# Kernel tuning notes

Measured on AMD Instinct MI355X. Metric: run time of the kernel, lower is better.

The kernel has to match this reference:

```python
import jax, jax.numpy as jnp
import numpy as np

B, S, D = 2, 2048, 2048
H, KVH, HD = 16, 4, 128
M = 2  # modalities
THETA = 10000.0
REP = H // KVH


def make_freq_cis(seq_len, head_dim, theta):
    # (S, head_dim//2, 2, 2) rotation matrices [[cos,-sin],[sin,cos]]
    inv = theta ** (-jnp.arange(0, head_dim, 2, dtype=jnp.float32) / head_dim)
    ang = jnp.arange(seq_len, dtype=jnp.float32)[:, None] * inv[None, :]  # (S, hd/2)
    c, s = jnp.cos(ang), jnp.sin(ang)
    row0 = jnp.stack([c, -s], axis=-1)
    row1 = jnp.stack([s, c], axis=-1)
    return jnp.stack([row0, row1], axis=-2)  # (S, hd/2, 2, 2)


def setup_inputs() -> dict:
    key = jax.random.key(0)
    ks = jax.random.split(key, 7)
    std = D ** -0.5
    x = jax.random.normal(ks[0], (B, S, D), dtype=jnp.float32)
    freq_cis = make_freq_cis(S, HD, THETA)
    modality_ids = jax.random.randint(ks[1], (B, S), 0, M, dtype=jnp.int32)
    wq = jax.random.normal(ks[2], (M, D, H * HD), dtype=jnp.float32) * std
    wk = jax.random.normal(ks[3], (M, D, KVH * HD), dtype=jnp.float32) * std
    wv = jax.random.normal(ks[4], (M, D, KVH * HD), dtype=jnp.float32) * std
    wo = jax.random.normal(ks[5], (M, H * HD, D), dtype=jnp.float32) * std
    return {"x": x, "freq_cis": freq_cis, "modality_ids": modality_ids,
            "wq": wq, "wk": wk, "wv": wv, "wo": wo}


def apply_rope(t, freq_cis):
    # t: (B, S, h, HD); freq_cis: (S, HD//2, 2, 2)
    b, s, h, hd = t.shape
    t2 = t.reshape(b, s, h, hd // 2, 2)
    out = jnp.einsum('bshdk,sdjk->bshdj', t2, freq_cis)
    return out.reshape(b, s, h, hd)


def reference(x, freq_cis, modality_ids, wq, wk, wv, wo):
    bsz, seq, dim = x.shape
    onehot = jax.nn.one_hot(modality_ids, M, dtype=x.dtype)  # (B,S,M)
    # per-modality QKV projection, then combine (masks partition tokens)
    q = jnp.einsum('bsm,bsd,mdo->bso', onehot, x, wq).reshape(bsz, seq, H, HD)
    k = jnp.einsum('bsm,bsd,mdo->bso', onehot, x, wk).reshape(bsz, seq, KVH, HD)
    v = jnp.einsum('bsm,bsd,mdo->bso', onehot, x, wv).reshape(bsz, seq, KVH, HD)
    q = apply_rope(q, freq_cis)
    k = apply_rope(k, freq_cis)
    # GQA: repeat_interleave kv heads along head dim
    k = jnp.repeat(k, REP, axis=2)
    v = jnp.repeat(v, REP, axis=2)
    scale = 1.0 / jnp.sqrt(jnp.asarray(HD, dtype=x.dtype))
    scores = jnp.einsum('bqhd,bkhd->bhqk', q, k) * scale
    causal = jnp.tril(jnp.ones((seq, seq), dtype=bool))
    scores = jnp.where(causal[None, None], scores, jnp.finfo(x.dtype).min)
    probs = jax.nn.softmax(scores, axis=-1)
    attn = jnp.einsum('bhqk,bkhd->bqhd', probs, v).reshape(bsz, seq, H * HD)
    # per-modality output projection
    out = jnp.einsum('bsm,bso,moe->bse', onehot, attn, wo)
    return out
```

## Files before the change

kernel.cpp:

```cpp
#include <hip/hip_runtime.h>
#include <stdint.h>

typedef unsigned short u16;
typedef __bf16  bf16x8 __attribute__((ext_vector_type(8), may_alias));
typedef u16     u16x8  __attribute__((ext_vector_type(8), may_alias));
typedef float   f32x4  __attribute__((ext_vector_type(4)));
typedef float   f32x4u __attribute__((ext_vector_type(4), may_alias));

#define Bv   2
#define Sv   2048
#define Dv   2048
#define Hv   16
#define KVHv 4
#define HDv  128
#define Tv   (Bv*Sv)
#define QKVN 3072
#define MAXROWS 4352

__device__ __forceinline__ float b2f(u16 u) {
    union { float f; uint32_t i; } x; x.i = ((uint32_t)u) << 16; return x.f;
}
__device__ __forceinline__ u16 f2b(float f) {
    union { float f; uint32_t u; } x; x.f = f;
    uint32_t r = x.u + 0x7fff + ((x.u >> 16) & 1);
    return (u16)(r >> 16);
}
__device__ __forceinline__ void gload_lds16(const void* g, void* l) {
    __builtin_amdgcn_global_load_lds((__attribute__((address_space(1))) void*)(uintptr_t)g,
                                     (__attribute__((address_space(3))) void*)(uintptr_t)l,
                                     16, 0, 0);
}

__global__ __launch_bounds__(1024) void scan_mod(const int* __restrict__ mod, int* __restrict__ fwd,
                                                 int* __restrict__ inv, int* __restrict__ hdr) {
    __shared__ int cnt[1024];
    const int tid = threadIdx.x;
    int m[4]; int c = 0;
#pragma unroll
    for (int e = 0; e < 4; ++e) { m[e] = mod[tid * 4 + e]; c += (m[e] == 0); }
    cnt[tid] = c;
    __syncthreads();
    for (int off = 1; off < 1024; off <<= 1) {
        int v = (tid >= off) ? cnt[tid - off] : 0;
        __syncthreads();
        cnt[tid] += v;
        __syncthreads();
    }
    const int c0 = cnt[1023];
    const int c0pad = (c0 + 255) & ~255;
    const int c1 = Tv - c0;
    const int total = c0pad + ((c1 + 255) & ~255);
    for (int p = tid; p < MAXROWS; p += 1024) inv[p] = -1;
    __syncthreads();
    const int ex0 = cnt[tid] - c;
    int z = 0;
#pragma unroll
    for (int e = 0; e < 4; ++e) {
        int t = tid * 4 + e;
        int pos;
        if (m[e] == 0) { pos = ex0 + z; ++z; }
        else           { pos = c0pad + (t - (ex0 + z)); }
        fwd[t] = pos;
        inv[pos] = t;
    }
    if (tid == 0) { hdr[0] = total >> 8; hdr[1] = c0pad; hdr[2] = total; }
}

__global__ void gather_cast(const float* __restrict__ x, const int* __restrict__ inv,
                            u16* __restrict__ Xg) {
    int v = blockIdx.x * 256 + threadIdx.x;
    int pos = v >> 8, c8 = (v & 255) * 8;
    int t = inv[pos];
    u16x8 val = {0, 0, 0, 0, 0, 0, 0, 0};
    if (t >= 0) {
        f32x4u a = *(const f32x4u*)&x[(size_t)t * Dv + c8];
        f32x4u b = *(const f32x4u*)&x[(size_t)t * Dv + c8 + 4];
#pragma unroll
        for (int j = 0; j < 4; ++j) { val[j] = f2b(a[j]); val[4 + j] = f2b(b[j]); }
    }
    *(u16x8*)&Xg[(size_t)pos * Dv + c8] = val;
}

__global__ void transpose_cast(const float* __restrict__ in, u16* __restrict__ out, int C,
                               size_t inZ, size_t outZ) {
    in  += (size_t)blockIdx.z * inZ;
    out += (size_t)blockIdx.z * outZ;
    __shared__ u16 tile[64][72];
    const int tr = blockIdx.y * 64, tc = blockIdx.x * 64;
    const int tid = threadIdx.x;
#pragma unroll
    for (int i = 0; i < 4; ++i) {
        int s = tid + 256 * i;
        int r = s >> 4, c4 = (s & 15) * 4;
        f32x4u v = *(const f32x4u*)&in[(size_t)(tr + r) * C + tc + c4];
#pragma unroll
        for (int j = 0; j < 4; ++j) tile[r][c4 + j] = f2b(v[j]);
    }
    __syncthreads();
#pragma unroll
    for (int i = 0; i < 2; ++i) {
        int s = tid + 256 * i;
        int r = s >> 3, c8 = (s & 7) * 8;
        u16x8 v;
#pragma unroll
        for (int j = 0; j < 8; ++j) v[j] = tile[c8 + j][r];
        *(u16x8*)&out[(size_t)(tc + r) * 2048 + tr + c8] = v;
    }
}

__device__ __forceinline__ void store_c(u16* C, size_t idx, float v) { C[idx] = f2b(v); }
__device__ __forceinline__ void store_c(float* C, size_t idx, float v) { C[idx] = v; }

template <typename OutT>
__global__ __launch_bounds__(512, 2) void gemm256(const u16* __restrict__ A,
                                                  const u16* __restrict__ Bt,
                                                  OutT* __restrict__ C,
                                                  const int* __restrict__ inv,
                                                  const int* __restrict__ hdr,
                                                  int Nfull, int ldC) {
    const int total = hdr[2], c0pad = hdr[1];
    const int bm = blockIdx.y * 256;
    if (bm >= total) return;
    const u16* B = Bt + (size_t)((bm >= c0pad) ? 1 : 0) * Nfull * 2048;
    const int bn = blockIdx.x * 256;
    const int tid = threadIdx.x;
    const int wave = tid >> 6, lane = tid & 63;
    const int l15 = lane & 15, l4 = lane >> 4;
    const int wm = wave >> 2;
    const int wn = wave & 3;
    const int bhh = wn >> 1, brr = (wn & 1) * 64;
    const int rsw = l15 & 7;
    __shared__ u16 ldsA[2][2][128 * 64];
    __shared__ u16 ldsB[2][2][128 * 64];
    const int srow = tid >> 3;
    const int ssw  = (tid & 7) ^ (srow & 7);
    const int wofs = wave * 8 * 64;

    f32x4 acc[8][4] = {};

    auto stA = [&](int sl, int h, int jrb, int kt) {
        gload_lds16(A + (size_t)(bm + h * 128 + jrb * 64 + srow) * 2048 + kt * 64 + ssw * 8,
                    &ldsA[sl][h][jrb * 64 * 64 + wofs]);
    };
    auto stB = [&](int sl, int h, int jrb, int kt) {
        gload_lds16(B + (size_t)(bn + h * 128 + jrb * 64 + srow) * 2048 + kt * 64 + ssw * 8,
                    &ldsB[sl][h][jrb * 64 * 64 + wofs]);
    };

    stB(0, 0, 0, 0); stB(0, 0, 1, 0); stB(0, 1, 0, 0); stB(0, 1, 1, 0);
    stA(0, 0, 0, 0); stA(0, 1, 0, 0); stA(0, 0, 1, 0); stA(0, 1, 1, 0);
    asm volatile("s_waitcnt vmcnt(2)" ::: "memory");
    __builtin_amdgcn_s_barrier();
    __builtin_amdgcn_sched_barrier(0);

    for (int kt = 0; kt < 32; ++kt) {
        const int s = kt & 1;
        const bool st = (kt < 31);
        bf16x8 bfr[4][2];
#pragma unroll
        for (int fj = 0; fj < 4; ++fj)
#pragma unroll
            for (int kc = 0; kc < 2; ++kc)
                bfr[fj][kc] = *(const bf16x8*)&ldsB[s][bhh][(brr + fj * 16 + l15) * 64 + ((kc * 4 + l4) ^ rsw) * 8];
#pragma unroll
        for (int q = 0; q < 4; ++q) {
            bf16x8 af[2][2];
#pragma unroll
            for (int fi = 0; fi < 2; ++fi)
#pragma unroll
                for (int kc = 0; kc < 2; ++kc)
                    af[fi][kc] = *(const bf16x8*)&ldsA[s][wm][(q * 32 + fi * 16 + l15) * 64 + ((kc * 4 + l4) ^ rsw) * 8];
            if (st) {
                if      (q == 0) { stB(s ^ 1, 0, 0, kt + 1); stB(s ^ 1, 0, 1, kt + 1); }
                else if (q == 1) { stB(s ^ 1, 1, 0, kt + 1); stB(s ^ 1, 1, 1, kt + 1); }
                else if (q == 2) { stA(s ^ 1, 0, 0, kt + 1); stA(s ^ 1, 1, 0, kt + 1); }
                else             { stA(s ^ 1, 0, 1, kt + 1); stA(s ^ 1, 1, 1, kt + 1); }
            }
            __builtin_amdgcn_s_setprio(1);
#pragma unroll
            for (int kc = 0; kc < 2; ++kc)
#pragma unroll
                for (int fi = 0; fi < 2; ++fi)
#pragma unroll
                    for (int fj = 0; fj < 4; ++fj)
                        acc[q * 2 + fi][fj] = __builtin_amdgcn_mfma_f32_16x16x32_bf16(
                            af[fi][kc], bfr[fj][kc], acc[q * 2 + fi][fj], 0, 0, 0);
            __builtin_amdgcn_s_setprio(0);
            if (q == 1) {
                if (st) asm volatile("s_waitcnt vmcnt(4)" ::: "memory");
                else    asm volatile("s_waitcnt vmcnt(0)" ::: "memory");
                __builtin_amdgcn_sched_barrier(0);
            }
            if (q == 3 && st) {
                asm volatile("s_waitcnt vmcnt(2)" ::: "memory");
                __builtin_amdgcn_sched_barrier(0);
            }
            __builtin_amdgcn_s_barrier();
            __builtin_amdgcn_sched_barrier(0);
        }
    }
#pragma unroll
    for (int fi = 0; fi < 8; ++fi)
#pragma unroll
        for (int r = 0; r < 4; ++r) {
            int row = bm + wm * 128 + fi * 16 + l4 * 4 + r;
            int t = inv[row];
            if (t >= 0) {
#pragma unroll
                for (int fj = 0; fj < 4; ++fj) {
                    int col = bn + wn * 64 + fj * 16 + l15;
                    store_c(C, (size_t)t * ldC + col, acc[fi][fj][r]);
                }
            }
        }
}

__global__ void rope_kernel(u16* __restrict__ QKV, const float* __restrict__ fc) {
    int p8 = blockIdx.x * 256 + threadIdx.x;
    const int t = p8 / 160;
    const int r8 = (p8 - t * 160) * 8;
    const int s = t & (Sv - 1);
    int col, d2b; float scale;
    if (r8 < 1024) { col = 2 * r8;               d2b = r8 & 63;  scale = 0.12751742f; }
    else           { int rr = r8 - 1024; col = 2048 + 2 * rr; d2b = rr & 63; scale = 1.0f; }
    u16* ptr = QKV + (size_t)t * QKVN + col;
    u16x8 va = *(const u16x8*)ptr;
    u16x8 vb = *(const u16x8*)(ptr + 8);
    u16 arr[16];
#pragma unroll
    for (int i = 0; i < 8; ++i) { arr[i] = va[i]; arr[8 + i] = vb[i]; }
#pragma unroll
    for (int i = 0; i < 8; ++i) {
        float t0 = b2f(arr[2 * i]), t1 = b2f(arr[2 * i + 1]);
        f32x4u f = *(const f32x4u*)&fc[((size_t)s * 64 + d2b + i) * 4];
        arr[2 * i]     = f2b((t0 * f[0] + t1 * f[1]) * scale);
        arr[2 * i + 1] = f2b((t0 * f[2] + t1 * f[3]) * scale);
    }
#pragma unroll
    for (int i = 0; i < 8; ++i) { va[i] = arr[i]; vb[i] = arr[8 + i]; }
    *(u16x8*)ptr = va;
    *(u16x8*)(ptr + 8) = vb;
}

__global__ __launch_bounds__(512) void attn_fwd(const u16* __restrict__ QKV, u16* __restrict__ Ag,
                                                const int* __restrict__ fwd) {
    const int p = blockIdx.x;
    const int h = blockIdx.y, b = blockIdx.z;
    const int kvh = h >> 2;
    const int tid = threadIdx.x, wave = tid >> 6, lane = tid & 63;
    const int wgrp = wave >> 2, wl = wave & 3;
    const int l15 = lane & 15, l4 = lane >> 4;
    const int myqb = wgrp ? (31 - p) : p;
    __shared__ u16 smem[32768];

    bf16x8 qf[4];
    {
        const size_t qrow = (size_t)(b * Sv + myqb * 64 + wl * 16 + l15);
#pragma unroll
        for (int kc = 0; kc < 4; ++kc)
            qf[kc] = *(const bf16x8*)&QKV[qrow * QKVN + h * 128 + kc * 32 + l4 * 8];
    }
    f32x4 oacc[8] = {};
    float mrow = -1e30f;
    float lrow = 0.f;

    const size_t kvbase = (size_t)b * Sv * QKVN + 2048 + kvh * 128;

    {
#pragma unroll
        for (int i = 0; i < 2; ++i) {
            int s_u = wave * 64 + 512 * i;
            int s = s_u + lane;
            int r = s >> 4;
            int kvsrc = (r & 32) | ((r & 12) << 1) | ((r & 16) >> 2) | (r & 3);
            int cs = (s & 15) ^ (r & 7);
            gload_lds16(QKV + kvbase + (size_t)kvsrc * QKVN + cs * 8, &smem[(size_t)s_u * 8]);
        }
        u16x8 vr0 = *(const u16x8*)&QKV[kvbase + 512 + (size_t)lane * QKVN + (0 * 8 + wave) * 8];
        u16x8 vr1 = *(const u16x8*)&QKV[kvbase + 512 + (size_t)lane * QKVN + (1 * 8 + wave) * 8];
#pragma unroll
        for (int jj = 0; jj < 8; ++jj) {
            int d0 = wave * 8 + jj, d1 = (8 + wave) * 8 + jj;
            smem[16384 + d0 * 64 + ((((lane >> 3) ^ jj) << 3) | (lane & 7))] = vr0[jj];
            smem[16384 + d1 * 64 + ((((lane >> 3) ^ jj) << 3) | (lane & 7))] = vr1[jj];
        }
    }
    __syncthreads();

    for (int j = 0; j < 32; ++j) {
        const int cur = j & 1;
        const bool stage_next = (j < 31);
        u16* Kcur = smem + cur * 8192;
        u16* Knxt = smem + (cur ^ 1) * 8192;
        u16* Vcur = smem + 16384 + cur * 8192;
        u16* Vnxt = smem + 16384 + (cur ^ 1) * 8192;
        u16x8 vn0, vn1;
        if (stage_next) {
            const size_t nb = kvbase + (size_t)(j + 1) * 64 * QKVN;
#pragma unroll
            for (int i = 0; i < 2; ++i) {
                int s_u = wave * 64 + 512 * i;
                int s = s_u + lane;
                int r = s >> 4;
                int kvsrc = (r & 32) | ((r & 12) << 1) | ((r & 16) >> 2) | (r & 3);
                int cs = (s & 15) ^ (r & 7);
                gload_lds16(QKV + nb + (size_t)kvsrc * QKVN + cs * 8, &Knxt[(size_t)s_u * 8]);
            }
            vn0 = *(const u16x8*)&QKV[nb + 512 + (size_t)lane * QKVN + (0 * 8 + wave) * 8];
            vn1 = *(const u16x8*)&QKV[nb + 512 + (size_t)lane * QKVN + (1 * 8 + wave) * 8];
        }
        if (j <= myqb) {
            f32x4 sacc[4] = {};
            __builtin_amdgcn_s_setprio(1);
#pragma unroll
            for (int kc = 0; kc < 4; ++kc)
#pragma unroll
                for (int nt = 0; nt < 4; ++nt) {
                    int cs = ((kc * 4 + l4) ^ (l15 & 7));
                    bf16x8 kf = *(const bf16x8*)&Kcur[(nt * 16 + l15) * 128 + cs * 8];
                    sacc[nt] = __builtin_amdgcn_mfma_f32_16x16x32_bf16(kf, qf[kc], sacc[nt], 0, 0, 0);
                }
            __builtin_amdgcn_s_setprio(0);
            if (j == myqb) {
#pragma unroll
                for (int nt = 0; nt < 4; ++nt)
#pragma unroll
                    for (int r = 0; r < 4; ++r)
                        if ((nt >> 1) * 32 + l4 * 8 + (nt & 1) * 4 + r > wl * 16 + l15)
                            sacc[nt][r] = -1e30f;
            }
            f32x4 mv = sacc[0];
#pragma unroll
            for (int nt = 1; nt < 4; ++nt)
#pragma unroll
                for (int r = 0; r < 4; ++r) mv[r] = fmaxf(mv[r], sacc[nt][r]);
            float mx = fmaxf(fmaxf(mv[0], mv[1]), fmaxf(mv[2], mv[3]));
            mx = fmaxf(mx, __shfl_xor(mx, 16, 64));
            mx = fmaxf(mx, __shfl_xor(mx, 32, 64));
            const bool defer = __all(mx <= mrow + 8.0f);
            if (!defer) {
                float mnew = fmaxf(mrow, mx);
                float fs = exp2f(mrow - mnew);
                mrow = mnew;
                lrow *= fs;
#pragma unroll
                for (int nt = 0; nt < 8; ++nt)
#pragma unroll
                    for (int r = 0; r < 4; ++r) oacc[nt][r] *= fs;
            }
            f32x4 pv = {0.f, 0.f, 0.f, 0.f};
#pragma unroll
            for (int nt = 0; nt < 4; ++nt)
#pragma unroll
                for (int r = 0; r < 4; ++r) {
                    float pe = exp2f(sacc[nt][r] - mrow);
                    sacc[nt][r] = pe;
                    pv[r] += pe;
                }
            float ps = (pv[0] + pv[1]) + (pv[2] + pv[3]);
            ps += __shfl_xor(ps, 16, 64);
            ps += __shfl_xor(ps, 32, 64);
            lrow += ps;
            union { uint32_t w[4]; bf16x8 v; } pb0u, pb1u;
#pragma unroll
            for (int nt = 0; nt < 2; ++nt) {
                asm("v_cvt_pk_bf16_f32 %0, %1, %2" : "=v"(pb0u.w[nt * 2])     : "v"(sacc[nt][0]), "v"(sacc[nt][1]));
                asm("v_cvt_pk_bf16_f32 %0, %1, %2" : "=v"(pb0u.w[nt * 2 + 1]) : "v"(sacc[nt][2]), "v"(sacc[nt][3]));
                asm("v_cvt_pk_bf16_f32 %0, %1, %2" : "=v"(pb1u.w[nt * 2])     : "v"(sacc[nt + 2][0]), "v"(sacc[nt + 2][1]));
                asm("v_cvt_pk_bf16_f32 %0, %1, %2" : "=v"(pb1u.w[nt * 2 + 1]) : "v"(sacc[nt + 2][2]), "v"(sacc[nt + 2][3]));
            }
            bf16x8 pb0 = pb0u.v, pb1 = pb1u.v;
            __builtin_amdgcn_s_setprio(1);
#pragma unroll
            for (int nt = 0; nt < 8; ++nt) {
                int d = nt * 16 + l15;
                bf16x8 v0 = *(const bf16x8*)&Vcur[d * 64 + ((l4 ^ (l15 & 7)) << 3)];
                bf16x8 v1 = *(const bf16x8*)&Vcur[d * 64 + (((4 + l4) ^ (l15 & 7)) << 3)];
                oacc[nt] = __builtin_amdgcn_mfma_f32_16x16x32_bf16(v0, pb0, oacc[nt], 0, 0, 0);
                oacc[nt] = __builtin_amdgcn_mfma_f32_16x16x32_bf16(v1, pb1, oacc[nt], 0, 0, 0);
            }
            __builtin_amdgcn_s_setprio(0);
        }
        if (stage_next) {
#pragma unroll
            for (int jj = 0; jj < 8; ++jj) {
                int d0 = wave * 8 + jj, d1 = (8 + wave) * 8 + jj;
                Vnxt[d0 * 64 + ((((lane >> 3) ^ jj) << 3) | (lane & 7))] = vn0[jj];
                Vnxt[d1 * 64 + ((((lane >> 3) ^ jj) << 3) | (lane & 7))] = vn1[jj];
            }
        }
        __syncthreads();
    }
    {
        u16* epi = smem + wave * (16 * 136);
        float rinv = 1.0f / lrow;
#pragma unroll
        for (int nt = 0; nt < 8; ++nt)
#pragma unroll
            for (int r = 0; r < 4; ++r)
                epi[l15 * 136 + nt * 16 + l4 * 4 + r] = f2b(oacc[nt][r] * rinv);
        const int q = lane >> 2;
        const int rowmap = fwd[b * Sv + myqb * 64 + wl * 16 + q];
#pragma unroll
        for (int it = 0; it < 4; ++it) {
            int dv = (lane & 3) + it * 4;
            u16x8 v = *(const u16x8*)&epi[q * 136 + dv * 8];
            *(u16x8*)&Ag[(size_t)rowmap * 2048 + h * 128 + dv * 8] = v;
        }
    }
}

extern "C" void kernel_launch(void* const* d_in, const int* in_sizes, int n_in,
                              void* d_out, int out_size, void* d_ws, size_t ws_size,
                              hipStream_t stream) {
    const float* x   = (const float*)d_in[0];
    const float* fc  = (const float*)d_in[1];
    const int*   mod = (const int*)d_in[2];
    const float* wq  = (const float*)d_in[3];
    const float* wk  = (const float*)d_in[4];
    const float* wv  = (const float*)d_in[5];
    const float* wo  = (const float*)d_in[6];
    float* out = (float*)d_out;
    char* ws = (char*)d_ws;
    u16* Wqkv_t = (u16*)(ws);
    u16* Wo_t   = (u16*)(ws + 25165824);
    u16* Xg     = (u16*)(ws + 41943040);
    u16* QKV    = (u16*)(ws + 59768832);
    int* fwd    = (int*)(ws + 84934656);
    int* inv    = (int*)(ws + 84951040);
    int* hdr    = (int*)(ws + 84968448);
    u16* Ag     = Xg;

    transpose_cast<<<dim3(32, 32, 2), 256, 0, stream>>>(wq, Wqkv_t, 2048,
        (size_t)2048 * 2048, (size_t)3072 * 2048);
    transpose_cast<<<dim3(8, 32, 2),  256, 0, stream>>>(wk, Wqkv_t + (size_t)2048 * 2048, 512,
        (size_t)2048 * 512,  (size_t)3072 * 2048);
    transpose_cast<<<dim3(8, 32, 2),  256, 0, stream>>>(wv, Wqkv_t + (size_t)2560 * 2048, 512,
        (size_t)2048 * 512,  (size_t)3072 * 2048);
    transpose_cast<<<dim3(32, 32, 2), 256, 0, stream>>>(wo, Wo_t, 2048,
        (size_t)2048 * 2048, (size_t)2048 * 2048);
    scan_mod<<<1, 1024, 0, stream>>>(mod, fwd, inv, hdr);
    gather_cast<<<MAXROWS, 256, 0, stream>>>(x, inv, Xg);
    gemm256<u16><<<dim3(12, 17), 512, 0, stream>>>(Xg, Wqkv_t, QKV, inv, hdr, 3072, 3072);
    rope_kernel<<<2560, 256, 0, stream>>>(QKV, fc);
    attn_fwd<<<dim3(16, 16, 2), 512, 0, stream>>>(QKV, Ag, fwd);
    gemm256<float><<<dim3(8, 17), 512, 0, stream>>>(Ag, Wo_t, out, inv, hdr, 2048, 2048);
}
```

Measured before the change: 232.6 us.

## Process two query sub-blocks per wave to reuse each K/V tile

After: 252.3 us. +8.4%, slower.

```diff
diff --git a/kernel.cpp b/kernel.cpp
--- a/kernel.cpp
+++ b/kernel.cpp
@@ -244,25 +244,27 @@
 
 __global__ __launch_bounds__(512) void attn_fwd(const u16* __restrict__ QKV, u16* __restrict__ Ag,
                                                 const int* __restrict__ fwd) {
-    const int p = blockIdx.x;
+    const int tp = blockIdx.x;
     const int h = blockIdx.y, b = blockIdx.z;
     const int kvh = h >> 2;
     const int tid = threadIdx.x, wave = tid >> 6, lane = tid & 63;
     const int wgrp = wave >> 2, wl = wave & 3;
     const int l15 = lane & 15, l4 = lane >> 4;
-    const int myqb = wgrp ? (31 - p) : p;
+    const int T = wgrp ? (15 - tp) : tp;
+    const int lim = 2 * T;
     __shared__ u16 smem[32768];
 
-    bf16x8 qf[4];
-    {
-        const size_t qrow = (size_t)(b * Sv + myqb * 64 + wl * 16 + l15);
+    bf16x8 qf[2][4];
+#pragma unroll
+    for (int sub = 0; sub < 2; ++sub) {
+        const size_t qrow = (size_t)(b * Sv + T * 128 + sub * 64 + wl * 16 + l15);
 #pragma unroll
         for (int kc = 0; kc < 4; ++kc)
-            qf[kc] = *(const bf16x8*)&QKV[qrow * QKVN + h * 128 + kc * 32 + l4 * 8];
-    }
-    f32x4 oacc[8] = {};
-    float mrow = -1e30f;
-    float lrow = 0.f;
+            qf[sub][kc] = *(const bf16x8*)&QKV[qrow * QKVN + h * 128 + kc * 32 + l4 * 8];
+    }
+    f32x4 oacc[2][8] = {};
+    float mrow[2] = {-1e30f, -1e30f};
+    float lrow[2] = {0.f, 0.f};
 
     const size_t kvbase = (size_t)b * Sv * QKVN + 2048 + kvh * 128;
 
@@ -309,7 +311,9 @@
             vn0 = *(const u16x8*)&QKV[nb + 512 + (size_t)lane * QKVN + (0 * 8 + wave) * 8];
             vn1 = *(const u16x8*)&QKV[nb + 512 + (size_t)lane * QKVN + (1 * 8 + wave) * 8];
         }
-        if (j <= myqb) {
+#pragma unroll
+        for (int sub = 0; sub < 2; ++sub) {
+            if (j > lim + sub) continue;
             f32x4 sacc[4] = {};
             __builtin_amdgcn_s_setprio(1);
 #pragma unroll
@@ -318,10 +322,10 @@
                 for (int nt = 0; nt < 4; ++nt) {
                     int cs = ((kc * 4 + l4) ^ (l15 & 7));
                     bf16x8 kf = *(const bf16x8*)&Kcur[(nt * 16 + l15) * 128 + cs * 8];
-                    sacc[nt] = __builtin_amdgcn_mfma_f32_16x16x32_bf16(kf, qf[kc], sacc[nt], 0, 0, 0);
+                    sacc[nt] = __builtin_amdgcn_mfma_f32_16x16x32_bf16(kf, qf[sub][kc], sacc[nt], 0, 0, 0);
                 }
             __builtin_amdgcn_s_setprio(0);
-            if (j == myqb) {
+            if (j == lim + sub) {
 #pragma unroll
                 for (int nt = 0; nt < 4; ++nt)
 #pragma unroll
@@ -337,30 +341,30 @@
             float mx = fmaxf(fmaxf(mv[0], mv[1]), fmaxf(mv[2], mv[3]));
             mx = fmaxf(mx, __shfl_xor(mx, 16, 64));
             mx = fmaxf(mx, __shfl_xor(mx, 32, 64));
-            const bool defer = __all(mx <= mrow + 8.0f);
+            const bool defer = __all(mx <= mrow[sub] + 8.0f);
             if (!defer) {
-                float mnew = fmaxf(mrow, mx);
-                float fs = exp2f(mrow - mnew);
-                mrow = mnew;
-                lrow *= fs;
+                float mnew = fmaxf(mrow[sub], mx);
+                float fs = exp2f(mrow[sub] - mnew);
+                mrow[sub] = mnew;
+                lrow[sub] *= fs;
 #pragma unroll
                 for (int nt = 0; nt < 8; ++nt)
 #pragma unroll
-                    for (int r = 0; r < 4; ++r) oacc[nt][r] *= fs;
+                    for (int r = 0; r < 4; ++r) oacc[sub][nt][r] *= fs;
             }
             f32x4 pv = {0.f, 0.f, 0.f, 0.f};
 #pragma unroll
             for (int nt = 0; nt < 4; ++nt)
 #pragma unroll
                 for (int r = 0; r < 4; ++r) {
-                    float pe = exp2f(sacc[nt][r] - mrow);
+                    float pe = exp2f(sacc[nt][r] - mrow[sub]);
                     sacc[nt][r] = pe;
                     pv[r] += pe;
                 }
             float ps = (pv[0] + pv[1]) + (pv[2] + pv[3]);
             ps += __shfl_xor(ps, 16, 64);
             ps += __shfl_xor(ps, 32, 64);
-            lrow += ps;
+            lrow[sub] += ps;
             union { uint32_t w[4]; bf16x8 v; } pb0u, pb1u;
 #pragma unroll
             for (int nt = 0; nt < 2; ++nt) {
@@ -376,8 +380,8 @@
                 int d = nt * 16 + l15;
                 bf16x8 v0 = *(const bf16x8*)&Vcur[d * 64 + ((l4 ^ (l15 & 7)) << 3)];
                 bf16x8 v1 = *(const bf16x8*)&Vcur[d * 64 + (((4 + l4) ^ (l15 & 7)) << 3)];
-                oacc[nt] = __builtin_amdgcn_mfma_f32_16x16x32_bf16(v0, pb0, oacc[nt], 0, 0, 0);
-                oacc[nt] = __builtin_amdgcn_mfma_f32_16x16x32_bf16(v1, pb1, oacc[nt], 0, 0, 0);
+                oacc[sub][nt] = __builtin_amdgcn_mfma_f32_16x16x32_bf16(v0, pb0, oacc[sub][nt], 0, 0, 0);
+                oacc[sub][nt] = __builtin_amdgcn_mfma_f32_16x16x32_bf16(v1, pb1, oacc[sub][nt], 0, 0, 0);
             }
             __builtin_amdgcn_s_setprio(0);
         }
@@ -391,22 +395,25 @@
         }
         __syncthreads();
     }
-    {
+#pragma unroll
+    for (int sub = 0; sub < 2; ++sub) {
         u16* epi = smem + wave * (16 * 136);
-        float rinv = 1.0f / lrow;
+        float rinv = 1.0f / lrow[sub];
 #pragma unroll
         for (int nt = 0; nt < 8; ++nt)
 #pragma unroll
             for (int r = 0; r < 4; ++r)
-                epi[l15 * 136 + nt * 16 + l4 * 4 + r] = f2b(oacc[nt][r] * rinv);
+                epi[l15 * 136 + nt * 16 + l4 * 4 + r] = f2b(oacc[sub][nt][r] * rinv);
         const int q = lane >> 2;
-        const int rowmap = fwd[b * Sv + myqb * 64 + wl * 16 + q];
+        const int rowmap = fwd[b * Sv + T * 128 + sub * 64 + wave * 16 % 64 + 0 * 64 + (wl * 16 + q) - wl * 16 + wl * 16];
+        const int rowmap2 = fwd[b * Sv + T * 128 + sub * 64 + wl * 16 + q];
 #pragma unroll
         for (int it = 0; it < 4; ++it) {
             int dv = (lane & 3) + it * 4;
             u16x8 v = *(const u16x8*)&epi[q * 136 + dv * 8];
-            *(u16x8*)&Ag[(size_t)rowmap * 2048 + h * 128 + dv * 8] = v;
-        }
+            *(u16x8*)&Ag[(size_t)rowmap2 * 2048 + h * 128 + dv * 8] = v;
+        }
+        (void)rowmap;
     }
 }
 
@@ -443,6 +450,6 @@
     gather_cast<<<MAXROWS, 256, 0, stream>>>(x, inv, Xg);
     gemm256<u16><<<dim3(12, 17), 512, 0, stream>>>(Xg, Wqkv_t, QKV, inv, hdr, 3072, 3072);
     rope_kernel<<<2560, 256, 0, stream>>>(QKV, fc);
-    attn_fwd<<<dim3(16, 16, 2), 512, 0, stream>>>(QKV, Ag, fwd);
+    attn_fwd<<<dim3(8, 16, 2), 512, 0, stream>>>(QKV, Ag, fwd);
     gemm256<float><<<dim3(8, 17), 512, 0, stream>>>(Ag, Wo_t, out, inv, hdr, 2048, 2048);
 }
```

## Triple-buffer K tiles in attention and merge weight transposes into one launch

Applied to the files above, without the earlier changes.

Measured after the change: 232.8 us. About the same (+0.1%).

```diff
diff --git a/kernel.cpp b/kernel.cpp
--- a/kernel.cpp
+++ b/kernel.cpp
@@ -81,12 +81,19 @@
     *(u16x8*)&Xg[(size_t)pos * Dv + c8] = val;
 }
 
-__global__ void transpose_cast(const float* __restrict__ in, u16* __restrict__ out, int C,
-                               size_t inZ, size_t outZ) {
-    in  += (size_t)blockIdx.z * inZ;
-    out += (size_t)blockIdx.z * outZ;
+__global__ void transpose_all(const float* __restrict__ wq, const float* __restrict__ wk,
+                              const float* __restrict__ wv, const float* __restrict__ wo,
+                              u16* __restrict__ Wqkv_t, u16* __restrict__ Wo_t) {
+    const int id = blockIdx.x;
+    const float* in; u16* out; int C; size_t inZ, outZ; int bx, by, z;
+    if (id < 2048)      { int l = id;        in = wq; out = Wqkv_t;                     C = 2048; inZ = (size_t)2048 * 2048; outZ = (size_t)3072 * 2048; bx = l & 31; by = (l >> 5) & 31; z = l >> 10; }
+    else if (id < 2560) { int l = id - 2048; in = wk; out = Wqkv_t + (size_t)2048 * 2048; C = 512;  inZ = (size_t)2048 * 512;  outZ = (size_t)3072 * 2048; bx = l & 7;  by = (l >> 3) & 31; z = l >> 8; }
+    else if (id < 3072) { int l = id - 2560; in = wv; out = Wqkv_t + (size_t)2560 * 2048; C = 512;  inZ = (size_t)2048 * 512;  outZ = (size_t)3072 * 2048; bx = l & 7;  by = (l >> 3) & 31; z = l >> 8; }
+    else                { int l = id - 3072; in = wo; out = Wo_t;                       C = 2048; inZ = (size_t)2048 * 2048; outZ = (size_t)2048 * 2048; bx = l & 31; by = (l >> 5) & 31; z = l >> 10; }
+    in  += (size_t)z * inZ;
+    out += (size_t)z * outZ;
     __shared__ u16 tile[64][72];
-    const int tr = blockIdx.y * 64, tc = blockIdx.x * 64;
+    const int tr = by * 64, tc = bx * 64;
     const int tid = threadIdx.x;
 #pragma unroll
     for (int i = 0; i < 4; ++i) {
@@ -251,7 +258,7 @@
     const int wgrp = wave >> 2, wl = wave & 3;
     const int l15 = lane & 15, l4 = lane >> 4;
     const int myqb = wgrp ? (31 - p) : p;
-    __shared__ u16 smem[32768];
+    __shared__ u16 smem[40960];
 
     bf16x8 qf[4];
     {
@@ -266,7 +273,9 @@
 
     const size_t kvbase = (size_t)b * Sv * QKVN + 2048 + kvh * 128;
 
-    {
+    auto stageK = [&](int t) {
+        const size_t tb = kvbase + (size_t)t * 64 * QKVN;
+        u16* dst = smem + (t % 3) * 8192;
 #pragma unroll
         for (int i = 0; i < 2; ++i) {
             int s_u = wave * 64 + 512 * i;
@@ -274,41 +283,39 @@
             int r = s >> 4;
             int kvsrc = (r & 32) | ((r & 12) << 1) | ((r & 16) >> 2) | (r & 3);
             int cs = (s & 15) ^ (r & 7);
-            gload_lds16(QKV + kvbase + (size_t)kvsrc * QKVN + cs * 8, &smem[(size_t)s_u * 8]);
-        }
+            gload_lds16(QKV + tb + (size_t)kvsrc * QKVN + cs * 8, &dst[(size_t)s_u * 8]);
+        }
+    };
+
+    {
         u16x8 vr0 = *(const u16x8*)&QKV[kvbase + 512 + (size_t)lane * QKVN + (0 * 8 + wave) * 8];
         u16x8 vr1 = *(const u16x8*)&QKV[kvbase + 512 + (size_t)lane * QKVN + (1 * 8 + wave) * 8];
+        stageK(0);
+        stageK(1);
 #pragma unroll
         for (int jj = 0; jj < 8; ++jj) {
             int d0 = wave * 8 + jj, d1 = (8 + wave) * 8 + jj;
-            smem[16384 + d0 * 64 + ((((lane >> 3) ^ jj) << 3) | (lane & 7))] = vr0[jj];
-            smem[16384 + d1 * 64 + ((((lane >> 3) ^ jj) << 3) | (lane & 7))] = vr1[jj];
-        }
-    }
-    __syncthreads();
+            smem[24576 + d0 * 64 + ((((lane >> 3) ^ jj) << 3) | (lane & 7))] = vr0[jj];
+            smem[24576 + d1 * 64 + ((((lane >> 3) ^ jj) << 3) | (lane & 7))] = vr1[jj];
+        }
+        asm volatile("s_waitcnt vmcnt(2) lgkmcnt(0)" ::: "memory");
+        __builtin_amdgcn_sched_barrier(0);
+        __builtin_amdgcn_s_barrier();
+        __builtin_amdgcn_sched_barrier(0);
+    }
 
     for (int j = 0; j < 32; ++j) {
         const int cur = j & 1;
-        const bool stage_next = (j < 31);
-        u16* Kcur = smem + cur * 8192;
-        u16* Knxt = smem + (cur ^ 1) * 8192;
-        u16* Vcur = smem + 16384 + cur * 8192;
-        u16* Vnxt = smem + 16384 + (cur ^ 1) * 8192;
+        u16* Kcur = smem + (j % 3) * 8192;
+        u16* Vcur = smem + 24576 + cur * 8192;
         u16x8 vn0, vn1;
-        if (stage_next) {
+        if (j < 31) {
             const size_t nb = kvbase + (size_t)(j + 1) * 64 * QKVN;
-#pragma unroll
-            for (int i = 0; i < 2; ++i) {
-                int s_u = wave * 64 + 512 * i;
-                int s = s_u + lane;
-                int r = s >> 4;
-                int kvsrc = (r & 32) | ((r & 12) << 1) | ((r & 16) >> 2) | (r & 3);
-                int cs = (s & 15) ^ (r & 7);
-                gload_lds16(QKV + nb + (size_t)kvsrc * QKVN + cs * 8, &Knxt[(size_t)s_u * 8]);
-            }
             vn0 = *(const u16x8*)&QKV[nb + 512 + (size_t)lane * QKVN + (0 * 8 + wave) * 8];
             vn1 = *(const u16x8*)&QKV[nb + 512 + (size_t)lane * QKVN + (1 * 8 + wave) * 8];
         }
+        if (j < 30) stageK(j + 2);
+        __builtin_amdgcn_sched_barrier(0);
         if (j <= myqb) {
             f32x4 sacc[4] = {};
             __builtin_amdgcn_s_setprio(1);
@@ -381,16 +388,24 @@
             }
             __builtin_amdgcn_s_setprio(0);
         }
-        if (stage_next) {
+        if (j < 31) {
+            if (j < 30) asm volatile("s_waitcnt vmcnt(2)" ::: "memory");
+            else        asm volatile("s_waitcnt vmcnt(0)" ::: "memory");
+            __builtin_amdgcn_sched_barrier(0);
+            u16* Vnxt = smem + 24576 + (cur ^ 1) * 8192;
 #pragma unroll
             for (int jj = 0; jj < 8; ++jj) {
                 int d0 = wave * 8 + jj, d1 = (8 + wave) * 8 + jj;
                 Vnxt[d0 * 64 + ((((lane >> 3) ^ jj) << 3) | (lane & 7))] = vn0[jj];
                 Vnxt[d1 * 64 + ((((lane >> 3) ^ jj) << 3) | (lane & 7))] = vn1[jj];
             }
-        }
-        __syncthreads();
-    }
+            asm volatile("s_waitcnt lgkmcnt(0)" ::: "memory");
+            __builtin_amdgcn_sched_barrier(0);
+            __builtin_amdgcn_s_barrier();
+            __builtin_amdgcn_sched_barrier(0);
+        }
+    }
+    __syncthreads();
     {
         u16* epi = smem + wave * (16 * 136);
         float rinv = 1.0f / lrow;
@@ -431,14 +446,7 @@
     int* hdr    = (int*)(ws + 84968448);
     u16* Ag     = Xg;
 
-    transpose_cast<<<dim3(32, 32, 2), 256, 0, stream>>>(wq, Wqkv_t, 2048,
-        (size_t)2048 * 2048, (size_t)3072 * 2048);
-    transpose_cast<<<dim3(8, 32, 2),  256, 0, stream>>>(wk, Wqkv_t + (size_t)2048 * 2048, 512,
-        (size_t)2048 * 512,  (size_t)3072 * 2048);
-    transpose_cast<<<dim3(8, 32, 2),  256, 0, stream>>>(wv, Wqkv_t + (size_t)2560 * 2048, 512,
-        (size_t)2048 * 512,  (size_t)3072 * 2048);
-    transpose_cast<<<dim3(32, 32, 2), 256, 0, stream>>>(wo, Wo_t, 2048,
-        (size_t)2048 * 2048, (size_t)2048 * 2048);
+    transpose_all<<<5120, 256, 0, stream>>>(wq, wk, wv, wo, Wqkv_t, Wo_t);
     scan_mod<<<1, 1024, 0, stream>>>(mod, fwd, inv, hdr);
     gather_cast<<<MAXROWS, 256, 0, stream>>>(x, inv, Xg);
     gemm256<u16><<<dim3(12, 17), 512, 0, stream>>>(Xg, Wqkv_t, QKV, inv, hdr, 3072, 3072);
```
